# Kernel optimization log

Measured on AMD Instinct MI355X. Metric: run time of the kernel, lower is better.

Reference implementation:

```python
import jax, jax.numpy as jnp
import numpy as np

NUM_USERS = 100000
NUM_ITEMS = 50000
HIDDEN = [256, 128, 64]
BATCH = 1024


def setup_inputs() -> dict:
    key = jax.random.key(0)
    ks = jax.random.split(key, 12)
    user_ids = jax.random.randint(ks[0], (BATCH,), 0, NUM_USERS, dtype=jnp.int32)
    item_ids = jax.random.randint(ks[1], (BATCH,), 0, NUM_ITEMS, dtype=jnp.int32)
    in_dim = NUM_USERS + NUM_ITEMS
    # Linear weights stored [in, out] for x @ W + b
    W1 = jax.random.normal(ks[2], (in_dim, HIDDEN[0]), dtype=jnp.float32) * 0.01
    b1 = jnp.zeros((HIDDEN[0],), dtype=jnp.float32)
    W2 = jax.random.normal(ks[3], (HIDDEN[0], HIDDEN[1]), dtype=jnp.float32) * 0.05
    b2 = jnp.zeros((HIDDEN[1],), dtype=jnp.float32)
    W3 = jax.random.normal(ks[4], (HIDDEN[1], HIDDEN[2]), dtype=jnp.float32) * 0.05
    b3 = jnp.zeros((HIDDEN[2],), dtype=jnp.float32)
    W4 = jax.random.normal(ks[5], (HIDDEN[2], 1), dtype=jnp.float32) * 0.05
    b4 = jnp.zeros((1,), dtype=jnp.float32)
    return {"user_ids": user_ids, "item_ids": item_ids,
            "W1": W1, "b1": b1, "W2": W2, "b2": b2,
            "W3": W3, "b3": b3, "W4": W4, "b4": b4}


def reference(user_ids, item_ids, W1, b1, W2, b2, W3, b3, W4, b4):
    # one_hot(user) @ W1[:NUM_USERS] + one_hot(item) @ W1[NUM_USERS:] == row gathers
    h = W1[user_ids] + W1[NUM_USERS + item_ids] + b1  # [B, 256]
    h = jax.nn.relu(h)
    h = jax.nn.relu(h @ W2 + b2)                       # [B, 128]
    h = jax.nn.relu(h @ W3 + b3)                       # [B, 64]
    return h @ W4 + b4                                 # [B, 1]
```

## Files before the change

### kernel.cpp

```cpp
#include <hip/hip_runtime.h>

#define NUM_USERS 100000
#define H1 256
#define H2 128
#define H3 64
#define BATCH 1024

__global__ __launch_bounds__(256) void mlp_row(
    const int* __restrict__ user_ids,
    const int* __restrict__ item_ids,
    const float* __restrict__ W1, const float* __restrict__ b1,
    const float* __restrict__ W2, const float* __restrict__ b2,
    const float* __restrict__ W3, const float* __restrict__ b3,
    const float* __restrict__ W4, const float* __restrict__ b4,
    float* __restrict__ out)
{
    __shared__ float h1[H1];
    __shared__ float h2[H2];
    __shared__ float h3[H3];
    __shared__ float res;

    const int t   = threadIdx.x;
    const int row = blockIdx.x;

    const int u  = user_ids[row];
    const int it = item_ids[row];

    {
        float v = W1[(size_t)u * H1 + t]
                + W1[(size_t)(NUM_USERS + it) * H1 + t]
                + b1[t];
        h1[t] = v > 0.f ? v : 0.f;
    }
    __syncthreads();

    if (t < H2) {
        float acc = b2[t];
        for (int k = 0; k < H1; ++k)
            acc += h1[k] * W2[k * H2 + t];
        h2[t] = acc > 0.f ? acc : 0.f;
    }
    __syncthreads();

    if (t < H3) {
        float acc = b3[t];
        for (int k = 0; k < H2; ++k)
            acc += h2[k] * W3[k * H3 + t];
        h3[t] = acc > 0.f ? acc : 0.f;
    }
    __syncthreads();

    if (t == 0) {
        float acc = b4[0];
        for (int k = 0; k < H3; ++k)
            acc += h3[k] * W4[k];
        res = acc;
    }
    __syncthreads();

    if (t < 64)
        out[row] = res;
}

extern "C" void kernel_launch(void* const* d_in, const int* in_sizes, int n_in,
                              void* d_out, int out_size, void* d_ws, size_t ws_size,
                              hipStream_t stream) {
    const int*   user_ids = (const int*)d_in[0];
    const int*   item_ids = (const int*)d_in[1];
    const float* W1 = (const float*)d_in[2];
    const float* b1 = (const float*)d_in[3];
    const float* W2 = (const float*)d_in[4];
    const float* b2 = (const float*)d_in[5];
    const float* W3 = (const float*)d_in[6];
    const float* b3 = (const float*)d_in[7];
    const float* W4 = (const float*)d_in[8];
    const float* b4 = (const float*)d_in[9];
    float* out = (float*)d_out;

    dim3 grid(BATCH);
    dim3 block(256);
    mlp_row<<<grid, block, 0, stream>>>(user_ids, item_ids,
                                        W1, b1, W2, b2, W3, b3, W4, b4, out);
}
```

Before: 210.9 us.

## Split MLP layer reductions across all threads with float4 loads and shuffle reductions

Rewrites layers 2-4 so all 256 threads take part. Each thread computes a partial dot product over a K-slice for four output columns, using float4 weight loads and padded shared memory. Partials are combined with wavefront xor-shuffles. The final output is summed from per-wave partials, which removes one barrier and the serial single-thread layer 4. The aim is to cut the idle lanes and long serial loops of the original per-row kernel, at the cost of more shuffle traffic and register use.

```diff
diff --git a/kernel.cpp b/kernel.cpp
--- a/kernel.cpp
+++ b/kernel.cpp
@@ -6,7 +6,18 @@
 #define H3 64
 #define BATCH 1024
 
-__global__ __launch_bounds__(256) void mlp_row(
+__device__ __forceinline__ float relu_(float x) { return x > 0.f ? x : 0.f; }
+
+__device__ __forceinline__ float4 sxor4(const float4 v, const int off) {
+    float4 r;
+    r.x = __shfl_xor(v.x, off, 64);
+    r.y = __shfl_xor(v.y, off, 64);
+    r.z = __shfl_xor(v.z, off, 64);
+    r.w = __shfl_xor(v.w, off, 64);
+    return r;
+}
+
+__global__ __launch_bounds__(256, 4) void mlp_row(
     const int* __restrict__ user_ids,
     const int* __restrict__ item_ids,
     const float* __restrict__ W1, const float* __restrict__ b1,
@@ -15,51 +26,134 @@
     const float* __restrict__ W4, const float* __restrict__ b4,
     float* __restrict__ out)
 {
-    __shared__ float h1[H1];
-    __shared__ float h2[H2];
-    __shared__ float h3[H3];
-    __shared__ float res;
+    __shared__ __align__(16) float h1s[H1 + (H1 / 32) * 4];
+    __shared__ __align__(16) float h2s[H2 + (H2 / 8) * 4];
+    __shared__ float wpart[4];
 
     const int t   = threadIdx.x;
+    const int wv  = t >> 6;
+    const int l   = t & 63;
     const int row = blockIdx.x;
+
+    const int q2 = (wv << 3) | (l & 7);
+    const int ke = l >> 3;
+    const int q3 = (wv << 2) | (l & 3);
+    const int kg = l >> 2;
+
+    const float4 b2q = ((const float4*)b2)[q2];
+    const float4 b3q = ((const float4*)b3)[q3];
+    const float4 w4q = ((const float4*)W4)[q3];
+    const float  b4s = b4[0];
 
     const int u  = user_ids[row];
     const int it = item_ids[row];
 
     {
-        float v = W1[(size_t)u * H1 + t]
-                + W1[(size_t)(NUM_USERS + it) * H1 + t]
-                + b1[t];
-        h1[t] = v > 0.f ? v : 0.f;
+        const float v = W1[(size_t)u * H1 + t]
+                      + W1[(size_t)(NUM_USERS + it) * H1 + t]
+                      + b1[t];
+        h1s[t + ((t >> 5) << 2)] = relu_(v);
     }
     __syncthreads();
 
-    if (t < H2) {
-        float acc = b2[t];
-        for (int k = 0; k < H1; ++k)
-            acc += h1[k] * W2[k * H2 + t];
-        h2[t] = acc > 0.f ? acc : 0.f;
+    float4 a0 = {0.f, 0.f, 0.f, 0.f}, a1 = {0.f, 0.f, 0.f, 0.f};
+    {
+        const float4* __restrict__ h1q = (const float4*)(h1s + ke * 36);
+        const float*  __restrict__ w2b = W2 + (size_t)(ke << 5) * H2 + (q2 << 2);
+        #pragma unroll
+        for (int i4 = 0; i4 < 8; ++i4) {
+            const float4 h  = h1q[i4];
+            const float4 wa = *(const float4*)(w2b + (size_t)(4 * i4    ) * H2);
+            const float4 wb = *(const float4*)(w2b + (size_t)(4 * i4 + 1) * H2);
+            const float4 wc = *(const float4*)(w2b + (size_t)(4 * i4 + 2) * H2);
+            const float4 wd = *(const float4*)(w2b + (size_t)(4 * i4 + 3) * H2);
+            a0.x = fmaf(h.x, wa.x, a0.x); a0.y = fmaf(h.x, wa.y, a0.y);
+            a0.z = fmaf(h.x, wa.z, a0.z); a0.w = fmaf(h.x, wa.w, a0.w);
+            a1.x = fmaf(h.y, wb.x, a1.x); a1.y = fmaf(h.y, wb.y, a1.y);
+            a1.z = fmaf(h.y, wb.z, a1.z); a1.w = fmaf(h.y, wb.w, a1.w);
+            a0.x = fmaf(h.z, wc.x, a0.x); a0.y = fmaf(h.z, wc.y, a0.y);
+            a0.z = fmaf(h.z, wc.z, a0.z); a0.w = fmaf(h.z, wc.w, a0.w);
+            a1.x = fmaf(h.w, wd.x, a1.x); a1.y = fmaf(h.w, wd.y, a1.y);
+            a1.z = fmaf(h.w, wd.z, a1.z); a1.w = fmaf(h.w, wd.w, a1.w);
+        }
+    }
+    float4 s2;
+    s2.x = a0.x + a1.x; s2.y = a0.y + a1.y;
+    s2.z = a0.z + a1.z; s2.w = a0.w + a1.w;
+    {
+        float4 r;
+        r = sxor4(s2,  8); s2.x += r.x; s2.y += r.y; s2.z += r.z; s2.w += r.w;
+        r = sxor4(s2, 16); s2.x += r.x; s2.y += r.y; s2.z += r.z; s2.w += r.w;
+        r = sxor4(s2, 32); s2.x += r.x; s2.y += r.y; s2.z += r.z; s2.w += r.w;
+    }
+    if (ke == 0) {
+        float4 hh;
+        hh.x = relu_(s2.x + b2q.x);
+        hh.y = relu_(s2.y + b2q.y);
+        hh.z = relu_(s2.z + b2q.z);
+        hh.w = relu_(s2.w + b2q.w);
+        const int c0 = q2 << 2;
+        *(float4*)&h2s[c0 + ((c0 >> 3) << 2)] = hh;
     }
     __syncthreads();
 
-    if (t < H3) {
-        float acc = b3[t];
-        for (int k = 0; k < H2; ++k)
-            acc += h2[k] * W3[k * H3 + t];
-        h3[t] = acc > 0.f ? acc : 0.f;
+    float4 c0a = {0.f, 0.f, 0.f, 0.f}, c1a = {0.f, 0.f, 0.f, 0.f};
+    {
+        const float4* __restrict__ h2q = (const float4*)(h2s + kg * 12);
+        const float*  __restrict__ w3b = W3 + (size_t)(kg << 3) * H3 + (q3 << 2);
+        const float4 hA = h2q[0];
+        const float4 hB = h2q[1];
+        const float4 wq0 = *(const float4*)(w3b            );
+        const float4 wq1 = *(const float4*)(w3b +     H3   );
+        const float4 wq2 = *(const float4*)(w3b + 2 * H3   );
+        const float4 wq3 = *(const float4*)(w3b + 3 * H3   );
+        const float4 wq4 = *(const float4*)(w3b + 4 * H3   );
+        const float4 wq5 = *(const float4*)(w3b + 5 * H3   );
+        const float4 wq6 = *(const float4*)(w3b + 6 * H3   );
+        const float4 wq7 = *(const float4*)(w3b + 7 * H3   );
+        c0a.x = fmaf(hA.x, wq0.x, c0a.x); c0a.y = fmaf(hA.x, wq0.y, c0a.y);
+        c0a.z = fmaf(hA.x, wq0.z, c0a.z); c0a.w = fmaf(hA.x, wq0.w, c0a.w);
+        c1a.x = fmaf(hA.y, wq1.x, c1a.x); c1a.y = fmaf(hA.y, wq1.y, c1a.y);
+        c1a.z = fmaf(hA.y, wq1.z, c1a.z); c1a.w = fmaf(hA.y, wq1.w, c1a.w);
+        c0a.x = fmaf(hA.z, wq2.x, c0a.x); c0a.y = fmaf(hA.z, wq2.y, c0a.y);
+        c0a.z = fmaf(hA.z, wq2.z, c0a.z); c0a.w = fmaf(hA.z, wq2.w, c0a.w);
+        c1a.x = fmaf(hA.w, wq3.x, c1a.x); c1a.y = fmaf(hA.w, wq3.y, c1a.y);
+        c1a.z = fmaf(hA.w, wq3.z, c1a.z); c1a.w = fmaf(hA.w, wq3.w, c1a.w);
+        c0a.x = fmaf(hB.x, wq4.x, c0a.x); c0a.y = fmaf(hB.x, wq4.y, c0a.y);
+        c0a.z = fmaf(hB.x, wq4.z, c0a.z); c0a.w = fmaf(hB.x, wq4.w, c0a.w);
+        c1a.x = fmaf(hB.y, wq5.x, c1a.x); c1a.y = fmaf(hB.y, wq5.y, c1a.y);
+        c1a.z = fmaf(hB.y, wq5.z, c1a.z); c1a.w = fmaf(hB.y, wq5.w, c1a.w);
+        c0a.x = fmaf(hB.z, wq6.x, c0a.x); c0a.y = fmaf(hB.z, wq6.y, c0a.y);
+        c0a.z = fmaf(hB.z, wq6.z, c0a.z); c0a.w = fmaf(hB.z, wq6.w, c0a.w);
+        c1a.x = fmaf(hB.w, wq7.x, c1a.x); c1a.y = fmaf(hB.w, wq7.y, c1a.y);
+        c1a.z = fmaf(hB.w, wq7.z, c1a.z); c1a.w = fmaf(hB.w, wq7.w, c1a.w);
+    }
+    float4 s3;
+    s3.x = c0a.x + c1a.x; s3.y = c0a.y + c1a.y;
+    s3.z = c0a.z + c1a.z; s3.w = c0a.w + c1a.w;
+    {
+        float4 r;
+        r = sxor4(s3,  4); s3.x += r.x; s3.y += r.y; s3.z += r.z; s3.w += r.w;
+        r = sxor4(s3,  8); s3.x += r.x; s3.y += r.y; s3.z += r.z; s3.w += r.w;
+        r = sxor4(s3, 16); s3.x += r.x; s3.y += r.y; s3.z += r.z; s3.w += r.w;
+        r = sxor4(s3, 32); s3.x += r.x; s3.y += r.y; s3.z += r.z; s3.w += r.w;
+    }
+    if (kg == 0) {
+        const float h30 = relu_(s3.x + b3q.x);
+        const float h31 = relu_(s3.y + b3q.y);
+        const float h32 = relu_(s3.z + b3q.z);
+        const float h33 = relu_(s3.w + b3q.w);
+        float pv = fmaf(h30, w4q.x,
+                   fmaf(h31, w4q.y,
+                   fmaf(h32, w4q.z, h33 * w4q.w)));
+        pv += __shfl_xor(pv, 1, 64);
+        pv += __shfl_xor(pv, 2, 64);
+        if (l == 0) wpart[wv] = pv;
     }
     __syncthreads();
 
-    if (t == 0) {
-        float acc = b4[0];
-        for (int k = 0; k < H3; ++k)
-            acc += h3[k] * W4[k];
-        res = acc;
-    }
-    __syncthreads();
-
-    if (t < 64)
-        out[row] = res;
+    if (t == 0)
+        out[row] = ((wpart[0] + wpart[1]) + (wpart[2] + wpart[3])) + b4s;
 }
 
 extern "C" void kernel_launch(void* const* d_in, const int* in_sizes, int n_in,
```

Measured after the change: 206.1 us. 2.3% less time.
